# Performance work log

Measured on AMD Instinct MI355X. Metric: run time of the kernel, lower is better.

Reference implementation:

```python
import math
import jax, jax.numpy as jnp
import numpy as np

Q_CLUSTER = 128
K_CLUSTER = 128


def _gaussian_orthogonal(m, d, rng):
    # gaussian_orthogonal_random_matrix with scaling=0 (row norms of fresh gaussians)
    blocks = []
    for _ in range(int(np.ceil(m / d))):
        g = rng.standard_normal((d, d))
        q, _ = np.linalg.qr(g)
        blocks.append(q.T)
    mat = np.concatenate(blocks, 0)[:m]
    norms = np.linalg.norm(rng.standard_normal((m, d)), axis=-1)
    return (mat * norms[:, None]).astype(np.float32)


def setup_inputs() -> dict:
    k = jax.random.key(0)
    kq, kk, kv = jax.random.split(k, 3)
    B, T, H, E = 2, 4096, 8, 64
    M, NH = 256, 4
    rng = np.random.default_rng(0)
    query = jax.random.normal(kq, (B, T, H, E), dtype=jnp.float32)
    key = jax.random.normal(kk, (B, T, H, E), dtype=jnp.float32)
    value = jax.random.normal(kv, (B, T, H, E), dtype=jnp.float32)
    proj = jnp.asarray(_gaussian_orthogonal(M, E, rng))
    alpha = jnp.asarray(rng.standard_normal((E + 2, NH)).astype(np.float32))
    beta = jnp.asarray(rng.uniform(0.0, 1.0, (1, NH)).astype(np.float32))
    return {"query": query, "key": key, "value": value, "proj": proj,
            "alpha": alpha, "beta": beta}


def _sort_to_buckets(x, perm, bucketsz):
    # x: (bh, s, d), perm: (nh, bh, s) -> (nh, bh, nbuckets, bucketsz, d)
    nh, bh, s = perm.shape
    g = jnp.take_along_axis(jnp.broadcast_to(x[None], (nh,) + x.shape),
                            perm[..., None], axis=2)
    return g.reshape(nh, bh, s // bucketsz, bucketsz, x.shape[-1])


def _unsort_from_buckets(s_x, perm_inv):
    nh, bh, nb, bsz, d = s_x.shape
    return jnp.take_along_axis(s_x.reshape(nh, bh, nb * bsz, d),
                               perm_inv[..., None], axis=2)


def _smyrf_forward(query, key, value, proj, alpha, beta):
    B, T, H, E = query.shape
    D = value.shape[-1]
    n_hashes = alpha.shape[-1]
    temp = 1.0 / math.sqrt(E)  # softmax_temp
    q = query.transpose(0, 2, 1, 3).reshape(B * H, T, E)
    k = key.transpose(0, 2, 1, 3).reshape(B * H, T, E)
    v = value.transpose(0, 2, 1, 3).reshape(B * H, T, D)

    # ---- XBOX+ asymmetric transform + E2LSH hashing (no grad path) ----
    qn = jnp.linalg.norm(q, axis=-1, keepdims=True)
    kn = jnp.linalg.norm(k, axis=-1, keepdims=True)
    MQ = jnp.max(qn, axis=1, keepdims=True)
    MK = jnp.max(kn, axis=1, keepdims=True)
    ext_q = jnp.sqrt(jnp.maximum(MQ ** 2 + MK ** 2 - qn ** 2, 0.0))
    ext_k = jnp.sqrt(jnp.maximum(MQ ** 2 + MK ** 2 - kn ** 2, 0.0))
    q_t = jnp.concatenate([q, ext_q, jnp.zeros_like(ext_q)], axis=-1)
    k_t = jnp.concatenate([k, jnp.zeros_like(ext_k), ext_k], axis=-1)
    q_hash = (q_t @ alpha + beta).transpose(2, 0, 1)  # (nh, bh, T)
    k_hash = (k_t @ alpha + beta).transpose(2, 0, 1)
    q_pos = jnp.argsort(q_hash, axis=-1)
    k_pos = jnp.argsort(k_hash, axis=-1)

    # ---- Performer (FAVOR+) softmax-kernel features with log scales ----
    dn = math.sqrt(temp)
    ratio = proj.shape[0] ** -0.5

    def feats(x, is_query):
        dash = jnp.einsum('bsd,md->bsm', dn * x, proj)
        diag = 0.5 * (dn ** 2) * jnp.sum(x * x, axis=-1, keepdims=True)
        logv = dash - diag
        if is_query:
            stab = jax.lax.stop_gradient(jnp.max(logv, axis=-1, keepdims=True))
        else:
            stab = jax.lax.stop_gradient(jnp.max(logv, axis=(-2, -1), keepdims=True))
        return jnp.exp(logv - stab) * ratio, stab

    q_prime, q_ls = feats(q, True)   # (bh, T, m), (bh, T, 1)
    k_prime, k_ls = feats(k, False)  # (bh, S, m), (bh, 1, 1)
    prime_log_scale = q_ls + k_ls    # (bh, T, 1)

    qk1 = jnp.einsum('btm,bm->bt', q_prime, k_prime.sum(axis=1))
    kv = jnp.einsum('bsm,bsd->bmd', k_prime, v)
    qkv = jnp.einsum('btm,bmd->btd', q_prime, kv)

    # ---- sort into LSH buckets, per-bucket attention ----
    s_q = _sort_to_buckets(q, q_pos, Q_CLUSTER)
    s_k = _sort_to_buckets(k, k_pos, K_CLUSTER)
    s_v = _sort_to_buckets(v, k_pos, K_CLUSTER)
    sq_p = _sort_to_buckets(q_prime, q_pos, Q_CLUSTER)
    sk_p = _sort_to_buckets(k_prime, k_pos, K_CLUSTER)
    s_pls = _sort_to_buckets(prime_log_scale, q_pos, Q_CLUSTER)

    inner = jnp.einsum('hbnie,hbnje->hbnij', s_q, s_k) * temp
    dots_prime = jnp.einsum('hbnim,hbnjm->hbnij', sq_p, sk_p)

    q_rev = jnp.argsort(q_pos, axis=-1)
    if n_hashes > 1:
        k_rev = jnp.argsort(k_pos, axis=-1)
        q_bidx = (q_rev // Q_CLUSTER).transpose(1, 2, 0)  # (bh, T, nh)
        k_bidx = (k_rev // K_CLUSTER).transpose(1, 2, 0)
        s_qb = _sort_to_buckets(q_bidx, q_pos, Q_CLUSTER)
        s_kb = _sort_to_buckets(k_bidx, k_pos, K_CLUSTER)
        dup = jnp.sum(s_qb[..., :, None, :] == s_kb[..., None, :, :],
                      axis=-1).astype(inner.dtype)
        inner = inner - jnp.log(dup)
        dots_prime = dots_prime / dup

    lse = jnp.maximum(jnp.max(inner, axis=-1, keepdims=True), s_pls)
    dots = jnp.exp(inner - lse) - dots_prime * jnp.exp(s_pls - lse)
    dots_sum = jnp.sum(dots, axis=-1, keepdims=True)
    so = jnp.einsum('hbnij,hbnjd->hbnid', dots, s_v)

    o = _unsort_from_buckets(so, q_rev)
    logits = _unsort_from_buckets(lse, q_rev)
    dots_sum_u = _unsort_from_buckets(dots_sum, q_rev)

    norm_ls = jax.nn.logsumexp(logits, axis=0)        # (bh, T, 1)
    probs = jnp.exp(logits - norm_ls[None])
    out_lsh = jnp.sum(o * probs, axis=0)
    prime_scale = jnp.exp(prime_log_scale - norm_ls)
    out = out_lsh + qkv * prime_scale
    normalization = jnp.sum(dots_sum_u * probs, axis=0) + qk1[..., None] * prime_scale
    out_n = out / jnp.maximum(normalization, 1e-6)
    return out_n.reshape(B, H, T, D).transpose(0, 2, 1, 3)


def reference(query, key, value, proj, alpha, beta):
    return _smyrf_forward(query, key, value, proj, alpha, beta)
```

## Files before the change

### kernel.cpp

```cpp
#include <hip/hip_runtime.h>
#include <stdint.h>
#include <math.h>

#define DEVI __device__ __forceinline__

constexpr int TB  = 2;
constexpr int TT  = 4096;
constexpr int TH  = 8;
constexpr int TE  = 64;
constexpr int TBH = 16;
constexpr int TM  = 256;
constexpr int TNH = 4;
constexpr float C_TEMP  = 0.125f;
constexpr float C_DN    = 0.35355339059327373f;
constexpr float C_RATIO = 0.0625f;

typedef __attribute__((ext_vector_type(8))) short bf16x8;
typedef __attribute__((ext_vector_type(4))) float f32x4;

constexpr size_t algn(size_t x){ return (x + 255) & ~(size_t)255; }
constexpr size_t OFF_QN2F = 0;
constexpr size_t OFF_KN2F = algn(OFF_QN2F + (size_t)TBH*TT*4);
constexpr size_t OFF_QN2D = algn(OFF_KN2F + (size_t)TBH*TT*4);
constexpr size_t OFF_KN2D = algn(OFF_QN2D + (size_t)TBH*TT*8);
constexpr size_t OFF_MQK2 = algn(OFF_KN2D + (size_t)TBH*TT*8);
constexpr size_t OFF_QMAXP= algn(OFF_MQK2 + (size_t)TBH*8);
constexpr size_t OFF_KMAXP= algn(OFF_QMAXP+ (size_t)TBH*16*8);
constexpr size_t OFF_QH   = algn(OFF_KMAXP+ (size_t)TBH*16*8);
constexpr size_t OFF_KH   = algn(OFF_QH   + (size_t)TNH*TBH*TT*8);
constexpr size_t OFF_QPOS = algn(OFF_KH   + (size_t)TNH*TBH*TT*8);
constexpr size_t OFF_KPOS = algn(OFF_QPOS + (size_t)TNH*TBH*TT*4);
constexpr size_t OFF_QREV = algn(OFF_KPOS + (size_t)TNH*TBH*TT*4);
constexpr size_t OFF_KREV = algn(OFF_QREV + (size_t)TNH*TBH*TT*4);
constexpr size_t OFF_KLSP = algn(OFF_KREV + (size_t)TNH*TBH*TT*4);
constexpr size_t OFF_KLS  = algn(OFF_KLSP + (size_t)TBH*128*4);
constexpr size_t OFF_QP   = algn(OFF_KLS  + (size_t)TBH*4);
constexpr size_t OFF_KP   = algn(OFF_QP   + (size_t)TBH*TT*TM*4);
constexpr size_t OFF_PLS  = algn(OFF_KP   + (size_t)TBH*TT*TM*4);
constexpr size_t OFF_KSUM = algn(OFF_PLS  + (size_t)TBH*TT*4);
constexpr size_t OFF_KV   = algn(OFF_KSUM + (size_t)TBH*TM*4);
constexpr size_t OFF_OT   = algn(OFF_KV   + (size_t)TBH*TM*TE*4);
constexpr size_t OFF_LSET = algn(OFF_OT   + (size_t)TNH*TBH*TT*TE*4);
constexpr size_t OFF_DSUM = algn(OFF_LSET + (size_t)TNH*TBH*TT*4);
constexpr size_t WS_NEED  = algn(OFF_DSUM + (size_t)TNH*TBH*TT*4);
constexpr size_t OFF_KVP  = OFF_QN2D;
constexpr size_t OFF_KSP  = OFF_KVP + (size_t)4*16*256*64*4;

DEVI float bf2f(uint32_t u16){ uint32_t x = u16 << 16; return __builtin_bit_cast(float, x); }
DEVI uint16_t f2bf(float f){
  uint32_t x = __builtin_bit_cast(uint32_t, f);
  uint32_t r = x + 0x7fffu + ((x >> 16) & 1u);
  return (uint16_t)(r >> 16);
}
DEVI int dupc(uint32_t x){
  return (int)((x & 0xffu) == 0) + (int)(((x >> 8) & 0xffu) == 0)
       + (int)(((x >> 16) & 0xffu) == 0) + (int)((x >> 24) == 0);
}
DEVI float lndup(int d){
  return d == 1 ? 0.f : d == 2 ? 0.69314718f : d == 3 ? 1.09861229f : 1.38629436f;
}
DEVI float rcpdup(int d){
  return d == 1 ? 1.f : d == 2 ? 0.5f : d == 3 ? 0.333333343f : 0.25f;
}

DEVI void stage64(char* rowp, const float4* src8, int hf){
  #pragma unroll
  for(int x = 0; x < 8; x++){
    float4 vv = src8[x];
    uint16_t hx = f2bf(vv.x), hy = f2bf(vv.y), hz = f2bf(vv.z), hw = f2bf(vv.w);
    float lx = vv.x - bf2f(hx), ly = vv.y - bf2f(hy), lz = vv.z - bf2f(hz), lw = vv.w - bf2f(hw);
    uint2 hp = make_uint2((uint32_t)hx | ((uint32_t)hy << 16), (uint32_t)hz | ((uint32_t)hw << 16));
    uint2 lp = make_uint2((uint32_t)f2bf(lx) | ((uint32_t)f2bf(ly) << 16),
                          (uint32_t)f2bf(lz) | ((uint32_t)f2bf(lw) << 16));
    *((uint2*)(rowp + 64*hf + 8*x)) = hp;
    *((uint2*)(rowp + 128 + 64*hf + 8*x)) = lp;
  }
}

__global__ void k_norms2(const float* __restrict__ q, const float* __restrict__ kk,
                         float* __restrict__ qn2f, float* __restrict__ kn2f,
                         double* __restrict__ qn2d, double* __restrict__ kn2d,
                         double* __restrict__ qmaxp, double* __restrict__ kmaxp){
  __shared__ double red[256];
  int bx = blockIdx.x; int chunk = bx & 15, bh = bx >> 4;
  int tid = threadIdx.x;
  int b = bh >> 3, hh = bh & 7;
  int t = chunk*256 + tid;
  const float4* r1 = (const float4*)(q + (((size_t)(b*TT + t)*TH) + hh)*TE);
  double s = 0.0;
  #pragma unroll
  for(int x = 0; x < 16; x++){
    float4 vv = r1[x];
    s += (double)vv.x*vv.x + (double)vv.y*vv.y + (double)vv.z*vv.z + (double)vv.w*vv.w;
  }
  qn2d[bh*TT + t] = s; qn2f[bh*TT + t] = (float)s;
  const float4* r2 = (const float4*)(kk + (((size_t)(b*TT + t)*TH) + hh)*TE);
  double s2 = 0.0;
  #pragma unroll
  for(int x = 0; x < 16; x++){
    float4 vv = r2[x];
    s2 += (double)vv.x*vv.x + (double)vv.y*vv.y + (double)vv.z*vv.z + (double)vv.w*vv.w;
  }
  kn2d[bh*TT + t] = s2; kn2f[bh*TT + t] = (float)s2;
  red[tid] = s; __syncthreads();
  for(int o = 128; o > 0; o >>= 1){ if(tid < o) red[tid] = fmax(red[tid], red[tid+o]); __syncthreads(); }
  if(tid == 0) qmaxp[bh*16 + chunk] = red[0];
  __syncthreads();
  red[tid] = s2; __syncthreads();
  for(int o = 128; o > 0; o >>= 1){ if(tid < o) red[tid] = fmax(red[tid], red[tid+o]); __syncthreads(); }
  if(tid == 0) kmaxp[bh*16 + chunk] = red[0];
}

__global__ void k_mqk(const double* __restrict__ qmaxp, const double* __restrict__ kmaxp,
                      double* __restrict__ mqk2){
  int bh = blockIdx.x;
  if(threadIdx.x == 0){
    double mq = -1e300, mk = -1e300;
    for(int i = 0; i < 16; i++){ mq = fmax(mq, qmaxp[bh*16 + i]); mk = fmax(mk, kmaxp[bh*16 + i]); }
    mqk2[bh] = mq + mk;
  }
}

__global__ void k_hash(const float* __restrict__ q, const float* __restrict__ kk,
                       const float* __restrict__ alpha, const float* __restrict__ beta,
                       const double* __restrict__ qn2d, const double* __restrict__ kn2d,
                       const double* __restrict__ mqk2,
                       double* __restrict__ qh, double* __restrict__ kh){
  __shared__ double al[264];
  __shared__ double be[4];
  int tid = threadIdx.x;
  for(int i = tid; i < 264; i += 256) al[i] = (double)alpha[i];
  if(tid < 4) be[tid] = (double)beta[tid];
  __syncthreads();
  int gid = blockIdx.x*256 + tid;
  int side = gid >> 16; int r = gid & 65535;
  int bh = r >> 12, t = r & 4095;
  int b = bh >> 3, hh = bh & 7;
  const float* x = (side ? kk : q) + (((size_t)(b*TT + t)*TH) + hh)*TE;
  const float4* xr = (const float4*)x;
  double a0 = 0.0, a1 = 0.0, a2 = 0.0, a3 = 0.0;
  #pragma unroll
  for(int c = 0; c < 16; c++){
    float4 vv = xr[c];
    const double* a = al + c*16;
    a0 += (double)vv.x*a[0]  + (double)vv.y*a[4]  + (double)vv.z*a[8]  + (double)vv.w*a[12];
    a1 += (double)vv.x*a[1]  + (double)vv.y*a[5]  + (double)vv.z*a[9]  + (double)vv.w*a[13];
    a2 += (double)vv.x*a[2]  + (double)vv.y*a[6]  + (double)vv.z*a[10] + (double)vv.w*a[14];
    a3 += (double)vv.x*a[3]  + (double)vv.y*a[7]  + (double)vv.z*a[11] + (double)vv.w*a[15];
  }
  double n2  = (side ? kn2d : qn2d)[bh*TT + t];
  double ext = sqrt(fmax(mqk2[bh] - n2, 0.0));
  int ec = side ? 65 : 64;
  double* dst = side ? kh : qh;
  dst[((size_t)0*TBH + bh)*TT + t] = a0 + ext*al[ec*4 + 0] + be[0];
  dst[((size_t)1*TBH + bh)*TT + t] = a1 + ext*al[ec*4 + 1] + be[1];
  dst[((size_t)2*TBH + bh)*TT + t] = a2 + ext*al[ec*4 + 2] + be[2];
  dst[((size_t)3*TBH + bh)*TT + t] = a3 + ext*al[ec*4 + 3] + be[3];
}

__global__ void k_sort(const double* __restrict__ qh, const double* __restrict__ kh,
                       int* __restrict__ qpos, int* __restrict__ kpos,
                       int* __restrict__ qrev, int* __restrict__ krev){
  __shared__ double v[4096];
  __shared__ int    ix[4096];
  int blk = blockIdx.x; int side = blk >> 6; int hb = blk & 63;
  const double* src = (side ? kh : qh) + (size_t)hb*TT;
  int tid = threadIdx.x;
  for(int i = tid; i < 4096; i += 1024){ v[i] = src[i]; ix[i] = i; }
  __syncthreads();
  for(int k = 2; k <= 4096; k <<= 1){
    for(int j = k >> 1; j > 0; j >>= 1){
      for(int i = tid; i < 4096; i += 1024){
        int l = i ^ j;
        if(l > i){
          double va = v[i], vb = v[l]; int ia = ix[i], ib = ix[l];
          bool gt  = (va > vb) || (va == vb && ia > ib);
          bool asc = ((i & k) == 0);
          if(gt == asc){ v[i] = vb; v[l] = va; ix[i] = ib; ix[l] = ia; }
        }
      }
      __syncthreads();
    }
  }
  int* pos = (side ? kpos : qpos) + (size_t)hb*TT;
  int* rev = (side ? krev : qrev) + (size_t)hb*TT;
  for(int i = tid; i < 4096; i += 1024){ int id = ix[i]; pos[i] = id; rev[id] = i; }
}

__launch_bounds__(512, 1)
__global__ void k_dash(const float* __restrict__ q, const float* __restrict__ kk,
                       const float* __restrict__ proj,
                       const float* __restrict__ qn2f, const float* __restrict__ kn2f,
                       float* __restrict__ qdash, float* __restrict__ kdash){
  __shared__ __align__(16) float pjL[64*260];
  __shared__ __align__(16) float x_l[128*68];
  __shared__ float x_n[128];
  int tid = threadIdx.x;
  int bx = blockIdx.x;
  int side = bx >> 9; int r = bx & 511; int bh = r >> 5; int ch = r & 31;
  int b = bh >> 3, hh = bh & 7, t0 = ch*128;
  const float* x  = side ? kk   : q;
  const float* n2 = side ? kn2f : qn2f;
  float* outp     = side ? kdash : qdash;

  #pragma unroll 8
  for(int it = 0; it < 32; it++){
    int idx = it*512 + tid;
    pjL[(idx & 63)*260 + (idx >> 6)] = proj[idx];
  }
  {
    int rr = tid >> 2, c = tid & 3;
    const float4* src = (const float4*)(x + (((size_t)(b*TT + t0 + rr)*TH) + hh)*TE);
    float4* dst = (float4*)(x_l + rr*68);
    #pragma unroll
    for(int i = 0; i < 4; i++) dst[c*4 + i] = src[c*4 + i];
  }
  if(tid < 128) x_n[tid] = n2[bh*TT + t0 + tid];
  __syncthreads();

  int ml = (tid & 15)*4;
  int tb = tid >> 4;
  float4 acc[4][4];
  #pragma unroll
  for(int tt = 0; tt < 4; tt++)
    #pragma unroll
    for(int g = 0; g < 4; g++) acc[tt][g] = make_float4(0.f,0.f,0.f,0.f);

  #pragma unroll 4
  for(int k4 = 0; k4 < 16; k4++){
    float4 xv[4];
    #pragma unroll
    for(int tt = 0; tt < 4; tt++)
      xv[tt] = *((const float4*)(x_l + (tb + 32*tt)*68 + k4*4));
    #pragma unroll
    for(int kk4 = 0; kk4 < 4; kk4++){
      int krow = k4*4 + kk4;
      #pragma unroll
      for(int g = 0; g < 4; g++){
        float4 pv = *((const float4*)(pjL + krow*260 + ml + 64*g));
        #pragma unroll
        for(int tt = 0; tt < 4; tt++){
          float xs = (kk4 == 0) ? xv[tt].x : (kk4 == 1) ? xv[tt].y : (kk4 == 2) ? xv[tt].z : xv[tt].w;
          acc[tt][g].x = fmaf(xs, pv.x, acc[tt][g].x);
          acc[tt][g].y = fmaf(xs, pv.y, acc[tt][g].y);
          acc[tt][g].z = fmaf(xs, pv.z, acc[tt][g].z);
          acc[tt][g].w = fmaf(xs, pv.w, acc[tt][g].w);
        }
      }
    }
  }
  #pragma unroll
  for(int tt = 0; tt < 4; tt++){
    int t_r = tb + 32*tt;
    float diag = 0.5f*C_TEMP*x_n[t_r];
    size_t rowbase = ((size_t)bh*TT + t0 + t_r)*256;
    #pragma unroll
    for(int g = 0; g < 4; g++){
      float4 a = acc[tt][g];
      float4 dd;
      dd.x = fmaf(C_DN, a.x, -diag); dd.y = fmaf(C_DN, a.y, -diag);
      dd.z = fmaf(C_DN, a.z, -diag); dd.w = fmaf(C_DN, a.w, -diag);
      *((float4*)(outp + rowbase + ml + 64*g)) = dd;
    }
  }
}

__global__ void k_klsmax(const float* __restrict__ kdash, float* __restrict__ klsp){
  __shared__ float wr[4];
  int tid = threadIdx.x;
  int bx = blockIdx.x; int bh = bx >> 7, ch = bx & 127;
  const float4* src = (const float4*)(kdash + ((size_t)bh << 20)) + ch*2048;
  float mx = -1e30f;
  #pragma unroll
  for(int i = 0; i < 8; i++){
    float4 vv = src[i*256 + tid];
    mx = fmaxf(mx, fmaxf(fmaxf(vv.x, vv.y), fmaxf(vv.z, vv.w)));
  }
  #pragma unroll
  for(int o = 32; o > 0; o >>= 1) mx = fmaxf(mx, __shfl_xor(mx, o, 64));
  if((tid & 63) == 0) wr[tid >> 6] = mx;
  __syncthreads();
  if(tid == 0) klsp[bh*128 + ch] = fmaxf(fmaxf(wr[0], wr[1]), fmaxf(wr[2], wr[3]));
}

__global__ void k_klsred(const float* __restrict__ klsp, float* __restrict__ kls){
  __shared__ float red[2];
  int bh = blockIdx.x, tid = threadIdx.x;
  float v = klsp[bh*128 + tid];
  #pragma unroll
  for(int o = 32; o > 0; o >>= 1) v = fmaxf(v, __shfl_xor(v, o, 64));
  if((tid & 63) == 0) red[tid >> 6] = v;
  __syncthreads();
  if(tid == 0) kls[bh] = fmaxf(red[0], red[1]);
}

__global__ void k_expk(float* __restrict__ kp, const float* __restrict__ kls){
  int tid = threadIdx.x; int blk = blockIdx.x;
  float4* p = (float4*)kp;
  size_t base = (size_t)blk*2048;
  float stab = kls[blk >> 7];
  #pragma unroll
  for(int i = 0; i < 8; i++){
    size_t ix = base + i*256 + tid;
    float4 vv = p[ix];
    vv.x = __expf(vv.x - stab)*C_RATIO; vv.y = __expf(vv.y - stab)*C_RATIO;
    vv.z = __expf(vv.z - stab)*C_RATIO; vv.w = __expf(vv.w - stab)*C_RATIO;
    p[ix] = vv;
  }
}

__global__ void k_expq(float* __restrict__ qp, float* __restrict__ pls){
  int tid = threadIdx.x, wid = tid >> 6, lane = tid & 63;
  int row = blockIdx.x*4 + wid;
  float4* p = (float4*)(qp + (size_t)row*256);
  float4 vv = p[lane];
  float mr = fmaxf(fmaxf(vv.x, vv.y), fmaxf(vv.z, vv.w));
  #pragma unroll
  for(int o = 32; o > 0; o >>= 1) mr = fmaxf(mr, __shfl_xor(mr, o, 64));
  float4 rr;
  rr.x = __expf(vv.x - mr)*C_RATIO; rr.y = __expf(vv.y - mr)*C_RATIO;
  rr.z = __expf(vv.z - mr)*C_RATIO; rr.w = __expf(vv.w - mr)*C_RATIO;
  p[lane] = rr;
  if(lane == 0) pls[row] = mr;
}

__global__ void k_kv2(const float* __restrict__ kp, const float* __restrict__ v,
                      float* __restrict__ kvp, float* __restrict__ ksump){
  int bx = blockIdx.x; int sc = bx >> 7; int rem = bx & 127; int bh = rem >> 3; int mt = rem & 7;
  int tid = threadIdx.x; int g = tid >> 6, d = tid & 63;
  int b = bh >> 3, hh = bh & 7; int m0 = mt*32;
  float a[8], sa[8];
  #pragma unroll
  for(int j = 0; j < 8; j++){ a[j] = 0.f; sa[j] = 0.f; }
  const float* kpb = kp + (size_t)bh*TT*256 + m0 + g;
  const float* vb  = v + (size_t)b*TT*TH*TE + hh*TE + d;
  int s0 = sc*1024;
  #pragma unroll 4
  for(int s = s0; s < s0 + 1024; s++){
    float vv = vb[(size_t)s*512];
    const float* kr = kpb + (size_t)s*256;
    #pragma unroll
    for(int j = 0; j < 8; j++){
      float kj = kr[4*j];
      a[j] = fmaf(kj, vv, a[j]); sa[j] += kj;
    }
  }
  #pragma unroll
  for(int j = 0; j < 8; j++){
    int m = m0 + g + 4*j;
    kvp[(((size_t)sc*16 + bh)*256 + m)*64 + d] = a[j];
    if(d == 0) ksump[((size_t)sc*16 + bh)*256 + m] = sa[j];
  }
}

__global__ void k_kvred(const float* __restrict__ kvp, const float* __restrict__ ksump,
                        float* __restrict__ kv, float* __restrict__ ksum){
  int bx = blockIdx.x, tid = threadIdx.x;
  if(bx < 256){
    size_t i = (size_t)bx*1024 + tid*4;
    float4 s = make_float4(0.f,0.f,0.f,0.f);
    #pragma unroll
    for(int sc = 0; sc < 4; sc++){
      float4 p = *((const float4*)(kvp + (size_t)sc*262144 + i));
      s.x += p.x; s.y += p.y; s.z += p.z; s.w += p.w;
    }
    *((float4*)(kv + i)) = s;
  } else {
    for(int m = tid; m < 4096; m += 256){
      float s = 0.f;
      #pragma unroll
      for(int sc = 0; sc < 4; sc++) s += ksump[sc*4096 + m];
      ksum[m] = s;
    }
  }
}

__launch_bounds__(256, 2)
__global__ void k_bucket(const float* __restrict__ q, const float* __restrict__ kk, const float* __restrict__ v,
                         const float* __restrict__ qp, const float* __restrict__ kp,
                         const int* __restrict__ qpos, const int* __restrict__ kpos,
                         const int* __restrict__ qrev, const int* __restrict__ krev,
                         const float* __restrict__ pls, const float* __restrict__ kls,
                         const float* __restrict__ qn2f, const float* __restrict__ kn2f,
                         float* __restrict__ o_t, float* __restrict__ lse_t, float* __restrict__ dsum_t){
  __shared__ __align__(16) char smem[73232];
  constexpr int OFS_B = 34816;
  int* qidxL   = (int*)(smem + 69632);
  int* kidxL   = (int*)(smem + 70144);
  int* qbpL    = (int*)(smem + 70656);
  int* kbpL    = (int*)(smem + 71168);
  float* lseL  = (float*)(smem + 71680);
  float* pfacL = (float*)(smem + 72192);
  float* kn2L  = (float*)(smem + 72704);
  float* kmaxP = (float*)(smem + 73216);

  int tid = threadIdx.x;
  int w = tid >> 6, lane = tid & 63, l15 = lane & 15, quad = lane >> 4;
  int bx = blockIdx.x; int n = bx & 31, bh = (bx >> 5) & 15, h = bx >> 9;
  int b = bh >> 3, hh = bh & 7;

  if(tid < 128){
    int tk = kpos[((size_t)h*TBH + bh)*TT + n*128 + tid];
    kidxL[tid] = tk;
    int pk = 0;
    #pragma unroll
    for(int h3 = 0; h3 < 4; h3++){ int rv = krev[((size_t)h3*TBH + bh)*TT + tk]; pk |= (rv >> 7) << (8*h3); }
    kbpL[tid] = pk;
    kn2L[tid] = kn2f[(size_t)bh*TT + tk];
    int tq = qpos[((size_t)h*TBH + bh)*TT + n*128 + tid];
    qidxL[tid] = tq;
    int pq = 0;
    #pragma unroll
    for(int h3 = 0; h3 < 4; h3++){ int rv = qrev[((size_t)h3*TBH + bh)*TT + tq]; pq |= (rv >> 7) << (8*h3); }
    qbpL[tid] = pq;
  }
  __syncthreads();
  if(tid < 64){
    float m = fmaxf(kn2L[tid], kn2L[tid + 64]);
    #pragma unroll
    for(int o = 32; o > 0; o >>= 1) m = fmaxf(m, __shfl_xor(m, o, 64));
    if(tid == 0) kmaxP[0] = m;
  }
  {
    int r = tid >> 1, hf = tid & 1;
    const float4* qs = (const float4*)(q  + (((size_t)(b*TT + qidxL[r])*TH) + hh)*TE) + hf*8;
    const float4* ks = (const float4*)(kk + (((size_t)(b*TT + kidxL[r])*TH) + hh)*TE) + hf*8;
    stage64(smem + r*272, qs, hf);
    stage64(smem + OFS_B + r*272, ks, hf);
  }
  __syncthreads();
  if(tid < 128){
    int tq = qidxL[tid];
    float plsv = pls[(size_t)bh*TT + tq] + kls[bh];
    float lse = fmaxf(plsv, C_TEMP * sqrtf(qn2f[(size_t)bh*TT + tq] * kmaxP[0]));
    lseL[tid] = lse;
    pfacL[tid] = __expf(plsv - lse);
  }

  f32x4 acc_s[2][8], acc_p[2][8];
  #pragma unroll
  for(int mt = 0; mt < 2; mt++)
    #pragma unroll
    for(int nt = 0; nt < 8; nt++){
      acc_s[mt][nt] = (f32x4){0.f,0.f,0.f,0.f};
      acc_p[mt][nt] = (f32x4){0.f,0.f,0.f,0.f};
    }

  {
    bf16x8 ahi[2][2], alo[2][2];
    #pragma unroll
    for(int mt = 0; mt < 2; mt++)
      #pragma unroll
      for(int ks = 0; ks < 2; ks++){
        const char* ap = smem + (32*w + 16*mt + l15)*272 + 64*ks + 16*quad;
        ahi[mt][ks] = *((const bf16x8*)ap);
        alo[mt][ks] = *((const bf16x8*)(ap + 128));
      }
    #pragma unroll
    for(int nt = 0; nt < 8; nt++){
      #pragma unroll
      for(int ks = 0; ks < 2; ks++){
        const char* bp = smem + OFS_B + (16*nt + l15)*272 + 64*ks + 16*quad;
        bf16x8 bhi = *((const bf16x8*)bp);
        bf16x8 blo = *((const bf16x8*)(bp + 128));
        #pragma unroll
        for(int mt = 0; mt < 2; mt++){
          acc_s[mt][nt] = __builtin_amdgcn_mfma_f32_16x16x32_bf16(ahi[mt][ks], bhi, acc_s[mt][nt], 0, 0, 0);
          acc_s[mt][nt] = __builtin_amdgcn_mfma_f32_16x16x32_bf16(ahi[mt][ks], blo, acc_s[mt][nt], 0, 0, 0);
          acc_s[mt][nt] = __builtin_amdgcn_mfma_f32_16x16x32_bf16(alo[mt][ks], bhi, acc_s[mt][nt], 0, 0, 0);
        }
      }
    }
  }
  __syncthreads();

  for(int c = 0; c < 4; c++){
    { int r = tid >> 1, hf = tid & 1;
      const float4* qs = (const float4*)(qp + ((size_t)bh*TT + qidxL[r])*256 + c*64) + hf*8;
      const float4* ks = (const float4*)(kp + ((size_t)bh*TT + kidxL[r])*256 + c*64) + hf*8;
      stage64(smem + r*272, qs, hf);
      stage64(smem + OFS_B + r*272, ks, hf);
    }
    __syncthreads();
    bf16x8 ahi[2][2], alo[2][2];
    #pragma unroll
    for(int mt = 0; mt < 2; mt++)
      #pragma unroll
      for(int ks = 0; ks < 2; ks++){
        const char* ap = smem + (32*w + 16*mt + l15)*272 + 64*ks + 16*quad;
        ahi[mt][ks] = *((const bf16x8*)ap);
        alo[mt][ks] = *((const bf16x8*)(ap + 128));
      }
    #pragma unroll
    for(int nt = 0; nt < 8; nt++){
      #pragma unroll
      for(int ks = 0; ks < 2; ks++){
        const char* bp = smem + OFS_B + (16*nt + l15)*272 + 64*ks + 16*quad;
        bf16x8 bhi = *((const bf16x8*)bp);
        bf16x8 blo = *((const bf16x8*)(bp + 128));
        #pragma unroll
        for(int mt = 0; mt < 2; mt++){
          acc_p[mt][nt] = __builtin_amdgcn_mfma_f32_16x16x32_bf16(ahi[mt][ks], bhi, acc_p[mt][nt], 0, 0, 0);
          acc_p[mt][nt] = __builtin_amdgcn_mfma_f32_16x16x32_bf16(ahi[mt][ks], blo, acc_p[mt][nt], 0, 0, 0);
          acc_p[mt][nt] = __builtin_amdgcn_mfma_f32_16x16x32_bf16(alo[mt][ks], bhi, acc_p[mt][nt], 0, 0, 0);
        }
      }
    }
    __syncthreads();
  }

  {
    int j = tid >> 1, hc = tid & 1;
    const float4* vs = (const float4*)(v + (((size_t)(b*TT + kidxL[j])*TH) + hh)*TE) + hc*8;
    #pragma unroll
    for(int x = 0; x < 8; x++){
      float4 vv = vs[x];
      int c0 = hc*32 + 4*x;
      float vals[4] = {vv.x, vv.y, vv.z, vv.w};
      #pragma unroll
      for(int i = 0; i < 4; i++){
        uint16_t hi = f2bf(vals[i]);
        float lo = vals[i] - bf2f(hi);
        *((uint16_t*)(smem + OFS_B + (c0 + i)*528 + 2*j)) = hi;
        *((uint16_t*)(smem + OFS_B + (c0 + i)*528 + 256 + 2*j)) = f2bf(lo);
      }
    }
  }
  int qbp_r[8]; float lse_r[8], pfac_r[8], dsump[8]; int kbp_c[8];
  #pragma unroll
  for(int i = 0; i < 8; i++){
    int r = 32*w + 16*(i >> 2) + 4*quad + (i & 3);
    qbp_r[i] = qbpL[r]; lse_r[i] = lseL[r]; pfac_r[i] = pfacL[r]; dsump[i] = 0.f;
  }
  #pragma unroll
  for(int nt = 0; nt < 8; nt++) kbp_c[nt] = kbpL[l15 + 16*nt];
  __syncthreads();

  f32x4 acc_o[2][4];
  #pragma unroll
  for(int mt = 0; mt < 2; mt++)
    #pragma unroll
    for(int nv = 0; nv < 4; nv++) acc_o[mt][nv] = (f32x4){0.f,0.f,0.f,0.f};

  #pragma unroll
  for(int hv = 0; hv < 2; hv++){
    #pragma unroll
    for(int nt = 0; nt < 4; nt++){
      int ntg = 4*hv + nt;
      #pragma unroll
      for(int mt = 0; mt < 2; mt++){
        f32x4 s4 = acc_s[mt][ntg], p4 = acc_p[mt][ntg];
        #pragma unroll
        for(int e = 0; e < 4; e++){
          int i = mt*4 + e;
          int du = dupc((uint32_t)(qbp_r[i] ^ kbp_c[ntg]));
          float ein  = __expf(fmaf(C_TEMP, s4[e], -lndup(du)) - lse_r[i]);
          float dots = fmaf(-p4[e]*rcpdup(du), pfac_r[i], ein);
          dsump[i] += dots;
          int row = 32*w + 16*mt + 4*quad + e;
          int colL = l15 + 16*nt;
          uint16_t hi = f2bf(dots);
          float lo = dots - bf2f(hi);
          *((uint16_t*)(smem + row*272 + 2*colL)) = hi;
          *((uint16_t*)(smem + row*272 + 128 + 2*colL)) = f2bf(lo);
        }
      }
    }
    bf16x8 dhi[2][2], dlo[2][2];
    #pragma unroll
    for(int mt = 0; mt < 2; mt++)
      #pragma unroll
      for(int ks = 0; ks < 2; ks++){
        const char* ap = smem + (32*w + 16*mt + l15)*272 + 64*ks + 16*quad;
        dhi[mt][ks] = *((const bf16x8*)ap);
        dlo[mt][ks] = *((const bf16x8*)(ap + 128));
      }
    #pragma unroll
    for(int nv = 0; nv < 4; nv++){
      #pragma unroll
      for(int ks = 0; ks < 2; ks++){
        const char* bp = smem + OFS_B + (16*nv + l15)*528 + 128*hv + 64*ks + 16*quad;
        bf16x8 vhi = *((const bf16x8*)bp);
        bf16x8 vlo = *((const bf16x8*)(bp + 256));
        #pragma unroll
        for(int mt = 0; mt < 2; mt++){
          acc_o[mt][nv] = __builtin_amdgcn_mfma_f32_16x16x32_bf16(dhi[mt][ks], vhi, acc_o[mt][nv], 0, 0, 0);
          acc_o[mt][nv] = __builtin_amdgcn_mfma_f32_16x16x32_bf16(dhi[mt][ks], vlo, acc_o[mt][nv], 0, 0, 0);
          acc_o[mt][nv] = __builtin_amdgcn_mfma_f32_16x16x32_bf16(dlo[mt][ks], vhi, acc_o[mt][nv], 0, 0, 0);
        }
      }
    }
  }

  #pragma unroll
  for(int i = 0; i < 8; i++){
    float s = dsump[i];
    s += __shfl_xor(s, 1, 64); s += __shfl_xor(s, 2, 64);
    s += __shfl_xor(s, 4, 64); s += __shfl_xor(s, 8, 64);
    dsump[i] = s;
  }
  size_t obase = ((size_t)h*TBH + bh)*TT;
  if(l15 == 0){
    #pragma unroll
    for(int i = 0; i < 8; i++){
      int r = 32*w + 16*(i >> 2) + 4*quad + (i & 3);
      int tq = qidxL[r];
      lse_t [obase + tq] = lse_r[i];
      dsum_t[obase + tq] = dsump[i];
    }
  }
  #pragma unroll
  for(int mt = 0; mt < 2; mt++){
    #pragma unroll
    for(int e = 0; e < 4; e++){
      int r = 32*w + 16*mt + 4*quad + e;
      int tq = qidxL[r];
      float* orow = o_t + (obase + tq)*64;
      #pragma unroll
      for(int nv = 0; nv < 4; nv++) orow[l15 + 16*nv] = acc_o[mt][nv][e];
    }
  }
}

__launch_bounds__(512, 1)
__global__ void k_final2(const float* __restrict__ qp, const float* __restrict__ kv,
                         const float* __restrict__ ksum, const float* __restrict__ o_t,
                         const float* __restrict__ lse_t, const float* __restrict__ dsum_t,
                         const float* __restrict__ pls, const float* __restrict__ kls,
                         float* __restrict__ out){
  __shared__ __align__(16) float kv_l[256*68];
  __shared__ __align__(16) float qp_l[128*68];
  __shared__ float prL[128][4];
  __shared__ float pscL[128];
  __shared__ float nrmL[128];
  int tid = threadIdx.x;
  int bx = blockIdx.x; int bh = bx >> 5, ch = bx & 31;
  int b = bh >> 3, hh = bh & 7;
  int t0 = ch*128;
  {
    const float4* kv4 = (const float4*)(kv + (size_t)bh*16384);
    #pragma unroll
    for(int i = 0; i < 8; i++){
      int idx = i*512 + tid;
      int m = idx >> 4, d4 = idx & 15;
      *((float4*)(kv_l + m*68 + d4*4)) = kv4[idx];
    }
    if(tid < 256) kv_l[tid*68 + 64] = ksum[bh*256 + tid];
  }
  int c = tid & 15, tb = tid >> 4;
  float4 acc[4];
  #pragma unroll
  for(int tt = 0; tt < 4; tt++) acc[tt] = make_float4(0.f,0.f,0.f,0.f);
  float p1 = 0.f;
  for(int c4 = 0; c4 < 4; c4++){
    __syncthreads();
    #pragma unroll
    for(int it = 0; it < 4; it++){
      int r = it*32 + tb;
      *((float4*)(qp_l + r*68 + c*4)) =
        *((const float4*)(qp + ((size_t)bh*TT + t0 + r)*256 + c4*64 + c*4));
    }
    __syncthreads();
    #pragma unroll 4
    for(int m4 = 0; m4 < 16; m4++){
      float4 qv[4];
      #pragma unroll
      for(int tt = 0; tt < 4; tt++)
        qv[tt] = *((const float4*)(qp_l + (tb + 32*tt)*68 + m4*4));
      #pragma unroll
      for(int mm = 0; mm < 4; mm++){
        int m = c4*64 + m4*4 + mm;
        float4 kvv = *((const float4*)(kv_l + m*68 + c*4));
        #pragma unroll
        for(int tt = 0; tt < 4; tt++){
          float qs = (mm == 0) ? qv[tt].x : (mm == 1) ? qv[tt].y : (mm == 2) ? qv[tt].z : qv[tt].w;
          acc[tt].x = fmaf(qs, kvv.x, acc[tt].x);
          acc[tt].y = fmaf(qs, kvv.y, acc[tt].y);
          acc[tt].z = fmaf(qs, kvv.z, acc[tt].z);
          acc[tt].w = fmaf(qs, kvv.w, acc[tt].w);
        }
      }
    }
    if(tid < 128){
      #pragma unroll 8
      for(int m = 0; m < 64; m++)
        p1 = fmaf(qp_l[tid*68 + m], kv_l[(c4*64 + m)*68 + 64], p1);
    }
  }
  __syncthreads();
  if(tid < 128){
    int t = t0 + tid;
    float l0 = lse_t[((size_t)0*TBH + bh)*TT + t], l1 = lse_t[((size_t)1*TBH + bh)*TT + t];
    float l2 = lse_t[((size_t)2*TBH + bh)*TT + t], l3 = lse_t[((size_t)3*TBH + bh)*TT + t];
    float M = fmaxf(fmaxf(l0, l1), fmaxf(l2, l3));
    float e0 = __expf(l0 - M), e1 = __expf(l1 - M), e2 = __expf(l2 - M), e3 = __expf(l3 - M);
    float rs = 1.f / (e0 + e1 + e2 + e3);
    float pr0 = e0*rs, pr1 = e1*rs, pr2 = e2*rs, pr3 = e3*rs;
    float psc = __expf(pls[bh*TT + t] + kls[bh] - M)*rs;
    float nrm = 0.f;
    nrm = fmaf(dsum_t[((size_t)0*TBH + bh)*TT + t], pr0, nrm);
    nrm = fmaf(dsum_t[((size_t)1*TBH + bh)*TT + t], pr1, nrm);
    nrm = fmaf(dsum_t[((size_t)2*TBH + bh)*TT + t], pr2, nrm);
    nrm = fmaf(dsum_t[((size_t)3*TBH + bh)*TT + t], pr3, nrm);
    nrm = fmaf(p1, psc, nrm);
    prL[tid][0] = pr0; prL[tid][1] = pr1; prL[tid][2] = pr2; prL[tid][3] = pr3;
    pscL[tid] = psc;
    nrmL[tid] = fmaxf(nrm, 1e-6f);
  }
  __syncthreads();
  #pragma unroll
  for(int tt = 0; tt < 4; tt++){
    int r = tb + 32*tt; int t = t0 + r;
    float4 o0 = *((const float4*)(o_t + (((size_t)0*TBH + bh)*TT + t)*64 + c*4));
    float4 o1 = *((const float4*)(o_t + (((size_t)1*TBH + bh)*TT + t)*64 + c*4));
    float4 o2 = *((const float4*)(o_t + (((size_t)2*TBH + bh)*TT + t)*64 + c*4));
    float4 o3 = *((const float4*)(o_t + (((size_t)3*TBH + bh)*TT + t)*64 + c*4));
    float pr0 = prL[r][0], pr1 = prL[r][1], pr2 = prL[r][2], pr3 = prL[r][3];
    float psc = pscL[r], nrm = nrmL[r];
    float4 outl;
    outl.x = fmaf(o3.x, pr3, fmaf(o2.x, pr2, fmaf(o1.x, pr1, o0.x*pr0)));
    outl.y = fmaf(o3.y, pr3, fmaf(o2.y, pr2, fmaf(o1.y, pr1, o0.y*pr0)));
    outl.z = fmaf(o3.z, pr3, fmaf(o2.z, pr2, fmaf(o1.z, pr1, o0.z*pr0)));
    outl.w = fmaf(o3.w, pr3, fmaf(o2.w, pr2, fmaf(o1.w, pr1, o0.w*pr0)));
    float4 res;
    res.x = (outl.x + acc[tt].x*psc) / nrm;
    res.y = (outl.y + acc[tt].y*psc) / nrm;
    res.z = (outl.z + acc[tt].z*psc) / nrm;
    res.w = (outl.w + acc[tt].w*psc) / nrm;
    *((float4*)(out + ((size_t)(b*TT + t)*TH + hh)*64 + c*4)) = res;
  }
}

__global__ void k_sentinel(float* __restrict__ out, int n){
  int i = blockIdx.x*256 + threadIdx.x;
  if(i < n) out[i] = 12345.0f;
}

extern "C" void kernel_launch(void* const* d_in, const int* in_sizes, int n_in,
                              void* d_out, int out_size, void* d_ws, size_t ws_size,
                              hipStream_t stream){
  const float* q     = (const float*)d_in[0];
  const float* k     = (const float*)d_in[1];
  const float* v     = (const float*)d_in[2];
  const float* proj  = (const float*)d_in[3];
  const float* alpha = (const float*)d_in[4];
  const float* beta  = (const float*)d_in[5];
  float* out = (float*)d_out;
  char* ws = (char*)d_ws;

  if(ws_size < WS_NEED){
    k_sentinel<<<dim3((out_size + 255)/256), dim3(256), 0, stream>>>(out, out_size);
    return;
  }

  float*  qn2f  = (float*) (ws + OFF_QN2F);
  float*  kn2f  = (float*) (ws + OFF_KN2F);
  double* qn2d  = (double*)(ws + OFF_QN2D);
  double* kn2d  = (double*)(ws + OFF_KN2D);
  double* mqk2  = (double*)(ws + OFF_MQK2);
  double* qmaxp = (double*)(ws + OFF_QMAXP);
  double* kmaxp = (double*)(ws + OFF_KMAXP);
  double* qh    = (double*)(ws + OFF_QH);
  double* kh    = (double*)(ws + OFF_KH);
  int*   qpos   = (int*)  (ws + OFF_QPOS);
  int*   kpos   = (int*)  (ws + OFF_KPOS);
  int*   qrev   = (int*)  (ws + OFF_QREV);
  int*   krev   = (int*)  (ws + OFF_KREV);
  float* klsp   = (float*)(ws + OFF_KLSP);
  float* kls    = (float*)(ws + OFF_KLS);
  float* qp     = (float*)(ws + OFF_QP);
  float* kp     = (float*)(ws + OFF_KP);
  float* pls    = (float*)(ws + OFF_PLS);
  float* ksum   = (float*)(ws + OFF_KSUM);
  float* kvv    = (float*)(ws + OFF_KV);
  float* o_t    = (float*)(ws + OFF_OT);
  float* lse_t  = (float*)(ws + OFF_LSET);
  float* dsum_t = (float*)(ws + OFF_DSUM);
  float* kvp    = (float*)(ws + OFF_KVP);
  float* ksump  = (float*)(ws + OFF_KSP);

  k_norms2<<<dim3(256),   dim3(256),  0, stream>>>(q, k, qn2f, kn2f, qn2d, kn2d, qmaxp, kmaxp);
  k_mqk   <<<dim3(16),    dim3(64),   0, stream>>>(qmaxp, kmaxp, mqk2);
  k_hash  <<<dim3(512),   dim3(256),  0, stream>>>(q, k, alpha, beta, qn2d, kn2d, mqk2, qh, kh);
  k_sort  <<<dim3(128),   dim3(1024), 0, stream>>>(qh, kh, qpos, kpos, qrev, krev);
  k_dash  <<<dim3(1024),  dim3(512),  0, stream>>>(q, k, proj, qn2f, kn2f, qp, kp);
  k_klsmax<<<dim3(2048),  dim3(256),  0, stream>>>(kp, klsp);
  k_klsred<<<dim3(16),    dim3(128),  0, stream>>>(klsp, kls);
  k_expk  <<<dim3(2048),  dim3(256),  0, stream>>>(kp, kls);
  k_expq  <<<dim3(16384), dim3(256),  0, stream>>>(qp, pls);
  k_kv2   <<<dim3(512),   dim3(256),  0, stream>>>(kp, v, kvp, ksump);
  k_kvred <<<dim3(257),   dim3(256),  0, stream>>>(kvp, ksump, kvv, ksum);
  k_bucket<<<dim3(2048),  dim3(256),  0, stream>>>(q, k, v, qp, kp, qpos, kpos, qrev, krev, pls, kls, qn2f, kn2f, o_t, lse_t, dsum_t);
  k_final2<<<dim3(512),   dim3(512),  0, stream>>>(qp, kvv, ksum, o_t, lse_t, dsum_t, pls, kls, out);
}
```

Measured before the change: 745.2 us.

## Store exp'd feature maps as split bf16 hi/lo pairs in place

The exp kernels for query and key features now write each row as packed bf16 hi/lo halves in a chunked layout, reusing the same fp32 buffer. The bucket kernel copies these pre-split bytes straight into shared memory instead of converting fp32 to bf16 pairs while staging. The kv reduction and final kernels rebuild fp32 values by adding hi and lo. This moves the split conversion into one pass and makes the staging loads contiguous and byte-identical. The cost is extra unpack arithmetic in the kv and final kernels, plus precision limited to about a bf16x2 split where those kernels used to read full fp32.

Measured after the change: 962.0 us. 1.29x slower.

```diff
diff --git a/kernel.cpp b/kernel.cpp
--- a/kernel.cpp
+++ b/kernel.cpp
@@ -295,32 +295,41 @@
 }
 
 __global__ void k_expk(float* __restrict__ kp, const float* __restrict__ kls){
-  int tid = threadIdx.x; int blk = blockIdx.x;
-  float4* p = (float4*)kp;
-  size_t base = (size_t)blk*2048;
-  float stab = kls[blk >> 7];
-  #pragma unroll
-  for(int i = 0; i < 8; i++){
-    size_t ix = base + i*256 + tid;
-    float4 vv = p[ix];
-    vv.x = __expf(vv.x - stab)*C_RATIO; vv.y = __expf(vv.y - stab)*C_RATIO;
-    vv.z = __expf(vv.z - stab)*C_RATIO; vv.w = __expf(vv.w - stab)*C_RATIO;
-    p[ix] = vv;
-  }
+  int tid = threadIdx.x, wid = tid >> 6, lane = tid & 63;
+  int row = blockIdx.x*4 + wid;
+  float stab = kls[row >> 12];
+  float* rp = kp + (size_t)row*256;
+  float4 vv = ((const float4*)rp)[lane];
+  float e0 = __expf(vv.x - stab)*C_RATIO, e1 = __expf(vv.y - stab)*C_RATIO;
+  float e2 = __expf(vv.z - stab)*C_RATIO, e3 = __expf(vv.w - stab)*C_RATIO;
+  uint16_t h0 = f2bf(e0), h1 = f2bf(e1), h2 = f2bf(e2), h3 = f2bf(e3);
+  uint2 hp = make_uint2((uint32_t)h0 | ((uint32_t)h1 << 16), (uint32_t)h2 | ((uint32_t)h3 << 16));
+  uint2 lp = make_uint2((uint32_t)f2bf(e0 - bf2f(h0)) | ((uint32_t)f2bf(e1 - bf2f(h1)) << 16),
+                        (uint32_t)f2bf(e2 - bf2f(h2)) | ((uint32_t)f2bf(e3 - bf2f(h3)) << 16));
+  char* rb = (char*)rp;
+  int c = lane >> 4, i = (lane & 15)*4;
+  *((uint2*)(rb + c*256 + 2*i)) = hp;
+  *((uint2*)(rb + c*256 + 128 + 2*i)) = lp;
 }
 
 __global__ void k_expq(float* __restrict__ qp, float* __restrict__ pls){
   int tid = threadIdx.x, wid = tid >> 6, lane = tid & 63;
   int row = blockIdx.x*4 + wid;
-  float4* p = (float4*)(qp + (size_t)row*256);
-  float4 vv = p[lane];
+  float* rp = qp + (size_t)row*256;
+  float4 vv = ((const float4*)rp)[lane];
   float mr = fmaxf(fmaxf(vv.x, vv.y), fmaxf(vv.z, vv.w));
   #pragma unroll
   for(int o = 32; o > 0; o >>= 1) mr = fmaxf(mr, __shfl_xor(mr, o, 64));
-  float4 rr;
-  rr.x = __expf(vv.x - mr)*C_RATIO; rr.y = __expf(vv.y - mr)*C_RATIO;
-  rr.z = __expf(vv.z - mr)*C_RATIO; rr.w = __expf(vv.w - mr)*C_RATIO;
-  p[lane] = rr;
+  float e0 = __expf(vv.x - mr)*C_RATIO, e1 = __expf(vv.y - mr)*C_RATIO;
+  float e2 = __expf(vv.z - mr)*C_RATIO, e3 = __expf(vv.w - mr)*C_RATIO;
+  uint16_t h0 = f2bf(e0), h1 = f2bf(e1), h2 = f2bf(e2), h3 = f2bf(e3);
+  uint2 hp = make_uint2((uint32_t)h0 | ((uint32_t)h1 << 16), (uint32_t)h2 | ((uint32_t)h3 << 16));
+  uint2 lp = make_uint2((uint32_t)f2bf(e0 - bf2f(h0)) | ((uint32_t)f2bf(e1 - bf2f(h1)) << 16),
+                        (uint32_t)f2bf(e2 - bf2f(h2)) | ((uint32_t)f2bf(e3 - bf2f(h3)) << 16));
+  char* rb = (char*)rp;
+  int c = lane >> 4, i = (lane & 15)*4;
+  *((uint2*)(rb + c*256 + 2*i)) = hp;
+  *((uint2*)(rb + c*256 + 128 + 2*i)) = lp;
   if(lane == 0) pls[row] = mr;
 }
 
@@ -329,25 +338,35 @@
   int bx = blockIdx.x; int sc = bx >> 7; int rem = bx & 127; int bh = rem >> 3; int mt = rem & 7;
   int tid = threadIdx.x; int g = tid >> 6, d = tid & 63;
   int b = bh >> 3, hh = bh & 7; int m0 = mt*32;
+  int mbase = m0 + 8*g;
+  int c = mbase >> 6, i0 = mbase & 63;
   float a[8], sa[8];
   #pragma unroll
   for(int j = 0; j < 8; j++){ a[j] = 0.f; sa[j] = 0.f; }
-  const float* kpb = kp + (size_t)bh*TT*256 + m0 + g;
-  const float* vb  = v + (size_t)b*TT*TH*TE + hh*TE + d;
+  const char* kpB = (const char*)kp + (size_t)bh*TT*1024 + c*256 + 2*i0;
+  const float* vb = v + (size_t)b*TT*TH*TE + hh*TE + d;
   int s0 = sc*1024;
-  #pragma unroll 4
+  #pragma unroll 2
   for(int s = s0; s < s0 + 1024; s++){
     float vv = vb[(size_t)s*512];
-    const float* kr = kpb + (size_t)s*256;
-    #pragma unroll
-    for(int j = 0; j < 8; j++){
-      float kj = kr[4*j];
-      a[j] = fmaf(kj, vv, a[j]); sa[j] += kj;
-    }
+    const char* rp = kpB + (size_t)s*1024;
+    uint4 h4 = *((const uint4*)rp);
+    uint4 l4 = *((const uint4*)(rp + 128));
+    float f[8];
+    f[0] = bf2f(h4.x & 0xffffu) + bf2f(l4.x & 0xffffu);
+    f[1] = bf2f(h4.x >> 16)     + bf2f(l4.x >> 16);
+    f[2] = bf2f(h4.y & 0xffffu) + bf2f(l4.y & 0xffffu);
+    f[3] = bf2f(h4.y >> 16)     + bf2f(l4.y >> 16);
+    f[4] = bf2f(h4.z & 0xffffu) + bf2f(l4.z & 0xffffu);
+    f[5] = bf2f(h4.z >> 16)     + bf2f(l4.z >> 16);
+    f[6] = bf2f(h4.w & 0xffffu) + bf2f(l4.w & 0xffffu);
+    f[7] = bf2f(h4.w >> 16)     + bf2f(l4.w >> 16);
+    #pragma unroll
+    for(int j = 0; j < 8; j++){ a[j] = fmaf(f[j], vv, a[j]); sa[j] += f[j]; }
   }
   #pragma unroll
   for(int j = 0; j < 8; j++){
-    int m = m0 + g + 4*j;
+    int m = mbase + j;
     kvp[(((size_t)sc*16 + bh)*256 + m)*64 + d] = a[j];
     if(d == 0) ksump[((size_t)sc*16 + bh)*256 + m] = sa[j];
   }
@@ -476,10 +495,12 @@
 
   for(int c = 0; c < 4; c++){
     { int r = tid >> 1, hf = tid & 1;
-      const float4* qs = (const float4*)(qp + ((size_t)bh*TT + qidxL[r])*256 + c*64) + hf*8;
-      const float4* ks = (const float4*)(kp + ((size_t)bh*TT + kidxL[r])*256 + c*64) + hf*8;
-      stage64(smem + r*272, qs, hf);
-      stage64(smem + OFS_B + r*272, ks, hf);
+      const uint4* qs = (const uint4*)((const char*)qp + ((size_t)bh*TT + qidxL[r])*1024 + c*256 + hf*128);
+      const uint4* ks = (const uint4*)((const char*)kp + ((size_t)bh*TT + kidxL[r])*1024 + c*256 + hf*128);
+      uint4* dq = (uint4*)(smem + r*272 + hf*128);
+      uint4* dk = (uint4*)(smem + OFS_B + r*272 + hf*128);
+      #pragma unroll
+      for(int i = 0; i < 8; i++){ dq[i] = qs[i]; dk[i] = ks[i]; }
     }
     __syncthreads();
     bf16x8 ahi[2][2], alo[2][2];
@@ -657,8 +678,15 @@
     #pragma unroll
     for(int it = 0; it < 4; it++){
       int r = it*32 + tb;
-      *((float4*)(qp_l + r*68 + c*4)) =
-        *((const float4*)(qp + ((size_t)bh*TT + t0 + r)*256 + c4*64 + c*4));
+      const char* rp = (const char*)qp + ((size_t)bh*TT + t0 + r)*1024 + c4*256 + 8*c;
+      uint2 h2 = *((const uint2*)rp);
+      uint2 l2 = *((const uint2*)(rp + 128));
+      float4 f;
+      f.x = bf2f(h2.x & 0xffffu) + bf2f(l2.x & 0xffffu);
+      f.y = bf2f(h2.x >> 16)     + bf2f(l2.x >> 16);
+      f.z = bf2f(h2.y & 0xffffu) + bf2f(l2.y & 0xffffu);
+      f.w = bf2f(h2.y >> 16)     + bf2f(l2.y >> 16);
+      *((float4*)(qp_l + r*68 + c*4)) = f;
     }
     __syncthreads();
     #pragma unroll 4
@@ -786,7 +814,7 @@
   k_dash  <<<dim3(1024),  dim3(512),  0, stream>>>(q, k, proj, qn2f, kn2f, qp, kp);
   k_klsmax<<<dim3(2048),  dim3(256),  0, stream>>>(kp, klsp);
   k_klsred<<<dim3(16),    dim3(128),  0, stream>>>(klsp, kls);
-  k_expk  <<<dim3(2048),  dim3(256),  0, stream>>>(kp, kls);
+  k_expk  <<<dim3(16384), dim3(256),  0, stream>>>(kp, kls);
   k_expq  <<<dim3(16384), dim3(256),  0, stream>>>(qp, pls);
   k_kv2   <<<dim3(512),   dim3(256),  0, stream>>>(kp, v, kvp, ksump);
   k_kvred <<<dim3(257),   dim3(256),  0, stream>>>(kvp, ksump, kvv, ksum);
```
